# Performance work log

Hardware: AMD Instinct MI355X
Metric: run time of the kernel (lower is better)

## Reference

```python
import jax, jax.numpy as jnp
import numpy as np

GROUP_SIZE = 128

def _dequant(q, s, zp):
    # q: [out, in] int values in [0, 2^bits); s, zp: [out, in//GROUP_SIZE]
    out_dim, in_dim = q.shape
    g = s.shape[1]
    qf = q.reshape(out_dim, g, GROUP_SIZE).astype(s.dtype)
    zf = zp[:, :, None].astype(s.dtype)
    return ((qf - zf) * s[:, :, None]).reshape(out_dim, in_dim)

def setup_inputs() -> dict:
    key = jax.random.key(0)
    ks = jax.random.split(key, 10)
    H, I = 4096, 11008
    T = 64  # decode-like token count -> weight-traffic bound
    gH, gI = H // GROUP_SIZE, I // GROUP_SIZE  # 32, 86
    x = jax.random.normal(ks[0], (T, H), dtype=jnp.float32)
    q1 = jax.random.randint(ks[1], (I, H), 0, 16, dtype=jnp.int32)
    s1 = jax.random.uniform(ks[2], (I, gH), dtype=jnp.float32) * 0.05
    zp1 = jax.random.randint(ks[3], (I, gH), 0, 16, dtype=jnp.int32)
    q3 = jax.random.randint(ks[4], (I, H), 0, 16, dtype=jnp.int32)
    s3 = jax.random.uniform(ks[5], (I, gH), dtype=jnp.float32) * 0.05
    zp3 = jax.random.randint(ks[6], (I, gH), 0, 16, dtype=jnp.int32)
    q2 = jax.random.randint(ks[7], (H, I), 0, 16, dtype=jnp.int32)
    s2 = jax.random.uniform(ks[8], (H, gI), dtype=jnp.float32) * 0.05
    zp2 = jax.random.randint(ks[9], (H, gI), 0, 16, dtype=jnp.int32)
    return {"x": x, "q1": q1, "s1": s1, "zp1": zp1, "q3": q3, "s3": s3,
            "zp3": zp3, "q2": q2, "s2": s2, "zp2": zp2}

def reference(x, q1, s1, zp1, q3, s3, zp3, q2, s2, zp2):
    w1 = _dequant(q1, s1, zp1)  # [I, H]
    w3 = _dequant(q3, s3, zp3)  # [I, H]
    w2 = _dequant(q2, s2, zp2)  # [H, I]
    x1 = x @ w1.T               # [T, I]
    x3 = x @ w3.T               # [T, I]
    x13 = jax.nn.silu(x1) * x3  # OPMX.silu(x1, x3): silu gate times up-proj
    return x13 @ w2.T           # [T, H]
```

## Files before the change

kernel.cpp:

```cpp
#include <hip/hip_runtime.h>
#include <hip/hip_fp16.h>

typedef _Float16 f16;
typedef f16 f16x8 __attribute__((ext_vector_type(8)));
typedef float f32x4 __attribute__((ext_vector_type(4)));

constexpr int T = 64;
constexpr int H = 4096;
constexpr int I = 11008;
constexpr int GH = 32;
constexpr int GI = 86;

__device__ __forceinline__ void gll16(const void* g, void* l) {
    __builtin_amdgcn_global_load_lds(
        (const __attribute__((address_space(1))) unsigned int*)g,
        (__attribute__((address_space(3))) unsigned int*)l, 16, 0, 0);
}

__device__ __forceinline__ f16x8 dq8v(int4 a, int4 b, float sv, float zv) {
    f16x8 r;
    auto p0 = __builtin_amdgcn_cvt_pkrtz((float)a.x * sv - zv, (float)a.y * sv - zv);
    auto p1 = __builtin_amdgcn_cvt_pkrtz((float)a.z * sv - zv, (float)a.w * sv - zv);
    auto p2 = __builtin_amdgcn_cvt_pkrtz((float)b.x * sv - zv, (float)b.y * sv - zv);
    auto p3 = __builtin_amdgcn_cvt_pkrtz((float)b.z * sv - zv, (float)b.w * sv - zv);
    r[0] = p0[0]; r[1] = p0[1]; r[2] = p1[0]; r[3] = p1[1];
    r[4] = p2[0]; r[5] = p2[1]; r[6] = p3[0]; r[7] = p3[1];
    return r;
}

__global__ __launch_bounds__(256) void k_cvt(const float* __restrict__ x,
                                             f16* __restrict__ xp) {
    int C = blockIdx.x * 256 + threadIdx.x;
    int w = C >> 8, m = (C >> 2) & 63, hi = C & 3;
    const float* src = x + (size_t)m * H + w * 32 + hi * 8;
    float4 a = *(const float4*)src;
    float4 b = *(const float4*)(src + 4);
    f16x8 o;
    o[0] = (f16)a.x; o[1] = (f16)a.y; o[2] = (f16)a.z; o[3] = (f16)a.w;
    o[4] = (f16)b.x; o[5] = (f16)b.y; o[6] = (f16)b.z; o[7] = (f16)b.w;
    *(f16x8*)(xp + (size_t)C * 8) = o;
}

__global__ __launch_bounds__(512, 4) void k_gateup(
    const f16* __restrict__ xp,
    const int* __restrict__ q1, const float* __restrict__ s1, const int* __restrict__ zp1,
    const int* __restrict__ q3, const float* __restrict__ s3, const int* __restrict__ zp3,
    float* __restrict__ part)
{
    __shared__ int tile[2 * 8192];
    const int t = threadIdx.x;
    const int wv = t >> 6, lane = t & 63, lo = lane & 15, hi = lane >> 4;
    const int mat = wv & 1, nsub = wv >> 1;
    const int R0 = blockIdx.x * 64;
    const int ks = blockIdx.y;
    const int brow = nsub * 16 + lo;
    const int grow = R0 + brow;
    const float* sm = mat ? s3 : s1;
    const int*   zm = mat ? zp3 : zp1;

    f32x4 acc[4] = {};

    for (int gl = 0; gl < 8; ++gl) {
        int g = ks * 8 + gl;
        float sv = sm[(size_t)grow * GH + g];
        float zv = (float)zm[(size_t)grow * GH + g] * sv;

        __syncthreads();
        #pragma unroll
        for (int k4 = 0; k4 < 4; ++k4) {
            int P = t + k4 * 512;
            int row = P >> 5, c = P & 31, cs = c ^ (row & 7);
            size_t gb = (size_t)(R0 + row) * (H * 4) + (size_t)g * 512 + cs * 16;
            int ldsi = (wv * 64 + k4 * 512) * 4;
            gll16((const char*)q1 + gb, (void*)&tile[ldsi]);
            gll16((const char*)q3 + gb, (void*)&tile[8192 + ldsi]);
        }
        asm volatile("s_waitcnt vmcnt(0)" ::: "memory");
        __syncthreads();

        #pragma unroll
        for (int w = 0; w < 4; ++w) {
            int cc = (w * 8 + hi * 2) ^ (brow & 7);
            int byte0 = mat * 32768 + (brow * 32 + cc) * 16;
            int4 b0 = *(const int4*)((const char*)tile + byte0);
            int4 b1 = *(const int4*)((const char*)tile + (byte0 ^ 16));
            f16x8 bf = dq8v(b0, b1, sv, zv);
            int wg = g * 4 + w;
            #pragma unroll
            for (int mt = 0; mt < 4; ++mt) {
                f16x8 af = *(const f16x8*)(xp + ((size_t)wg * 256 + (mt * 16 + lo) * 4 + hi) * 8);
                acc[mt] = __builtin_amdgcn_mfma_f32_16x16x32_f16(af, bf, acc[mt], 0, 0, 0);
            }
        }
    }

    float* pb = part + (size_t)(ks * 2 + mat) * T * I;
    #pragma unroll
    for (int mt = 0; mt < 4; ++mt)
        #pragma unroll
        for (int j = 0; j < 4; ++j)
            pb[(size_t)(mt * 16 + hi * 4 + j) * I + R0 + brow] = acc[mt][j];
}

__global__ __launch_bounds__(256) void k_comb(const float* __restrict__ part,
                                              f16* __restrict__ hp) {
    int C = blockIdx.x * 256 + threadIdx.x;
    int w = C >> 8, m = (C >> 2) & 63, hi = C & 3;
    int col = w * 32 + hi * 8;
    float ga[8] = {}, ua[8] = {};
    #pragma unroll
    for (int ks = 0; ks < 4; ++ks) {
        const float* pg = part + ((size_t)(ks * 2 + 0) * T + m) * I + col;
        const float* pu = part + ((size_t)(ks * 2 + 1) * T + m) * I + col;
        float4 g0 = *(const float4*)pg, g1 = *(const float4*)(pg + 4);
        float4 u0 = *(const float4*)pu, u1 = *(const float4*)(pu + 4);
        ga[0] += g0.x; ga[1] += g0.y; ga[2] += g0.z; ga[3] += g0.w;
        ga[4] += g1.x; ga[5] += g1.y; ga[6] += g1.z; ga[7] += g1.w;
        ua[0] += u0.x; ua[1] += u0.y; ua[2] += u0.z; ua[3] += u0.w;
        ua[4] += u1.x; ua[5] += u1.y; ua[6] += u1.z; ua[7] += u1.w;
    }
    f16x8 o;
    #pragma unroll
    for (int j = 0; j < 8; ++j) {
        float gv = ga[j];
        o[j] = (f16)(gv / (1.f + __expf(-gv)) * ua[j]);
    }
    *(f16x8*)(hp + (size_t)C * 8) = o;
}

__global__ __launch_bounds__(512, 4) void k_down(
    const f16* __restrict__ hp,
    const int* __restrict__ q2, const float* __restrict__ s2, const int* __restrict__ zp2,
    float* __restrict__ part2)
{
    __shared__ int tile[8192];
    __shared__ float xs[4][64][17];
    const int t = threadIdx.x;
    const int wv = t >> 6, lane = t & 63, lo = lane & 15, hi = lane >> 4;
    const int nsub = wv & 3, kh = wv >> 2;
    const int R0 = blockIdx.x * 64;
    const int y = blockIdx.y;
    const int g0 = (y * GI) >> 3, g1 = ((y + 1) * GI) >> 3;
    const int brow = nsub * 16 + lo;
    const int grow = R0 + brow;

    f32x4 acc[4] = {};

    for (int g = g0; g < g1; ++g) {
        float sv = s2[(size_t)grow * GI + g];
        float zv = (float)zp2[(size_t)grow * GI + g] * sv;

        __syncthreads();
        #pragma unroll
        for (int k4 = 0; k4 < 4; ++k4) {
            int P = t + k4 * 512;
            int row = P >> 5, c = P & 31, cs = c ^ (row & 7);
            size_t gb = (size_t)(R0 + row) * ((size_t)I * 4) + (size_t)g * 512 + cs * 16;
            gll16((const char*)q2 + gb, (void*)&tile[(wv * 64 + k4 * 512) * 4]);
        }
        asm volatile("s_waitcnt vmcnt(0)" ::: "memory");
        __syncthreads();

        #pragma unroll
        for (int ww = 0; ww < 2; ++ww) {
            int w = kh * 2 + ww;
            int cc = (w * 8 + hi * 2) ^ (brow & 7);
            int byte0 = (brow * 32 + cc) * 16;
            int4 b0 = *(const int4*)((const char*)tile + byte0);
            int4 b1 = *(const int4*)((const char*)tile + (byte0 ^ 16));
            f16x8 bf = dq8v(b0, b1, sv, zv);
            int wg = g * 4 + w;
            #pragma unroll
            for (int mt = 0; mt < 4; ++mt) {
                f16x8 af = *(const f16x8*)(hp + ((size_t)wg * 256 + (mt * 16 + lo) * 4 + hi) * 8);
                acc[mt] = __builtin_amdgcn_mfma_f32_16x16x32_f16(af, bf, acc[mt], 0, 0, 0);
            }
        }
    }

    __syncthreads();
    if (kh == 1) {
        #pragma unroll
        for (int mt = 0; mt < 4; ++mt)
            #pragma unroll
            for (int j = 0; j < 4; ++j)
                xs[nsub][mt * 16 + hi * 4 + j][lo] = acc[mt][j];
    }
    __syncthreads();
    if (kh == 0) {
        float* pb = part2 + (size_t)y * T * H;
        #pragma unroll
        for (int mt = 0; mt < 4; ++mt)
            #pragma unroll
            for (int j = 0; j < 4; ++j) {
                int m = mt * 16 + hi * 4 + j;
                pb[(size_t)m * H + R0 + brow] = acc[mt][j] + xs[nsub][m][lo];
            }
    }
}

__global__ __launch_bounds__(256) void k_red(const float* __restrict__ part2,
                                             float* __restrict__ out) {
    int i = (blockIdx.x * 256 + threadIdx.x) * 4;
    float4 s = {0.f, 0.f, 0.f, 0.f};
    #pragma unroll
    for (int y = 0; y < 8; ++y) {
        float4 v = *(const float4*)(part2 + (size_t)y * T * H + i);
        s.x += v.x; s.y += v.y; s.z += v.z; s.w += v.w;
    }
    *(float4*)(out + i) = s;
}

extern "C" void kernel_launch(void* const* d_in, const int* in_sizes, int n_in,
                              void* d_out, int out_size, void* d_ws, size_t ws_size,
                              hipStream_t stream) {
    const float* x   = (const float*)d_in[0];
    const int*   q1  = (const int*)d_in[1];
    const float* s1  = (const float*)d_in[2];
    const int*   zp1 = (const int*)d_in[3];
    const int*   q3  = (const int*)d_in[4];
    const float* s3  = (const float*)d_in[5];
    const int*   zp3 = (const int*)d_in[6];
    const int*   q2  = (const int*)d_in[7];
    const float* s2  = (const float*)d_in[8];
    const int*   zp2 = (const int*)d_in[9];

    char* ws = (char*)d_ws;
    f16*   xp    = (f16*)ws;
    f16*   hp    = (f16*)(ws + 524288);
    float* part  = (float*)(ws + 524288 + 1409024);
    float* part2 = (float*)(ws + 524288 + 1409024 + 22544384);

    k_cvt<<<128, 256, 0, stream>>>(x, xp);
    k_gateup<<<dim3(172, 4), 512, 0, stream>>>(xp, q1, s1, zp1, q3, s3, zp3, part);
    k_comb<<<344, 256, 0, stream>>>(part, hp);
    k_down<<<dim3(64, 8), 512, 0, stream>>>(hp, q2, s2, zp2, part2);
    k_red<<<256, 256, 0, stream>>>(part2, (float*)d_out);
}
```

Measured before the change: 171.8 us.

## Double-buffer weight tiles and split gate/up matrices across grid blocks

Both GEMM kernels now use two LDS buffers so the global-to-LDS load of the next group's weights is issued before the current group is dequantized and multiplied, with a partial vmcnt wait in place of a full drain. Gate and up projections move to separate blocks along a new grid z dimension, and blocks shrink from 512 to 256 threads. The activation fragments for a whole group are preloaded into registers. In k_down the intra-block K split and its LDS reduction are removed. The cost is more registers and LDS per block and fewer waves per block. In k_down each block now does more serial work per output tile.

```diff
diff --git a/kernel.cpp b/kernel.cpp
--- a/kernel.cpp
+++ b/kernel.cpp
@@ -41,57 +41,77 @@
     *(f16x8*)(xp + (size_t)C * 8) = o;
 }
 
-__global__ __launch_bounds__(512, 4) void k_gateup(
+template<int KDIM>
+__device__ __forceinline__ void stage_tile(const int* __restrict__ q, int R0, int g,
+                                           int* buf) {
+    const int t = threadIdx.x;
+    #pragma unroll
+    for (int k4 = 0; k4 < 8; ++k4) {
+        int P = t + k4 * 256;
+        int row = P >> 5, c = P & 31, cs = c ^ (row & 7);
+        size_t gb = (size_t)(R0 + row) * ((size_t)KDIM * 4) + (size_t)g * 512 + cs * 16;
+        gll16((const char*)q + gb, (void*)&buf[((t >> 6) * 64 + k4 * 256) * 4]);
+    }
+}
+
+__global__ __launch_bounds__(256, 2) void k_gateup(
     const f16* __restrict__ xp,
     const int* __restrict__ q1, const float* __restrict__ s1, const int* __restrict__ zp1,
     const int* __restrict__ q3, const float* __restrict__ s3, const int* __restrict__ zp3,
     float* __restrict__ part)
 {
-    __shared__ int tile[2 * 8192];
+    __shared__ int tile[2][8192];
     const int t = threadIdx.x;
     const int wv = t >> 6, lane = t & 63, lo = lane & 15, hi = lane >> 4;
-    const int mat = wv & 1, nsub = wv >> 1;
     const int R0 = blockIdx.x * 64;
     const int ks = blockIdx.y;
-    const int brow = nsub * 16 + lo;
+    const int mat = blockIdx.z;
+    const int brow = wv * 16 + lo;
     const int grow = R0 + brow;
+
+    const int*   q  = mat ? q3 : q1;
     const float* sm = mat ? s3 : s1;
     const int*   zm = mat ? zp3 : zp1;
 
     f32x4 acc[4] = {};
+    int cur = 0;
+
+    stage_tile<H>(q, R0, ks * 8, tile[0]);
 
     for (int gl = 0; gl < 8; ++gl) {
         int g = ks * 8 + gl;
         float sv = sm[(size_t)grow * GH + g];
         float zv = (float)zm[(size_t)grow * GH + g] * sv;
 
-        __syncthreads();
-        #pragma unroll
-        for (int k4 = 0; k4 < 4; ++k4) {
-            int P = t + k4 * 512;
-            int row = P >> 5, c = P & 31, cs = c ^ (row & 7);
-            size_t gb = (size_t)(R0 + row) * (H * 4) + (size_t)g * 512 + cs * 16;
-            int ldsi = (wv * 64 + k4 * 512) * 4;
-            gll16((const char*)q1 + gb, (void*)&tile[ldsi]);
-            gll16((const char*)q3 + gb, (void*)&tile[8192 + ldsi]);
-        }
-        asm volatile("s_waitcnt vmcnt(0)" ::: "memory");
-        __syncthreads();
-
+        f16x8 areg[16];
+        #pragma unroll
+        for (int w = 0; w < 4; ++w)
+            #pragma unroll
+            for (int mt = 0; mt < 4; ++mt)
+                areg[w * 4 + mt] = *(const f16x8*)(xp +
+                    ((size_t)(g * 4 + w) * 256 + (mt * 16 + lo) * 4 + hi) * 8);
+        asm volatile("" ::: "memory");
+
+        int gn = (gl < 7) ? g + 1 : g;
+        stage_tile<H>(q, R0, gn, tile[cur ^ 1]);
+
+        asm volatile("s_waitcnt vmcnt(8)" ::: "memory");
+        __syncthreads();
+
+        const char* tb = (const char*)tile[cur];
         #pragma unroll
         for (int w = 0; w < 4; ++w) {
             int cc = (w * 8 + hi * 2) ^ (brow & 7);
-            int byte0 = mat * 32768 + (brow * 32 + cc) * 16;
-            int4 b0 = *(const int4*)((const char*)tile + byte0);
-            int4 b1 = *(const int4*)((const char*)tile + (byte0 ^ 16));
+            int byte0 = (brow * 32 + cc) * 16;
+            int4 b0 = *(const int4*)(tb + byte0);
+            int4 b1 = *(const int4*)(tb + (byte0 ^ 16));
             f16x8 bf = dq8v(b0, b1, sv, zv);
-            int wg = g * 4 + w;
-            #pragma unroll
-            for (int mt = 0; mt < 4; ++mt) {
-                f16x8 af = *(const f16x8*)(xp + ((size_t)wg * 256 + (mt * 16 + lo) * 4 + hi) * 8);
-                acc[mt] = __builtin_amdgcn_mfma_f32_16x16x32_f16(af, bf, acc[mt], 0, 0, 0);
-            }
+            #pragma unroll
+            for (int mt = 0; mt < 4; ++mt)
+                acc[mt] = __builtin_amdgcn_mfma_f32_16x16x32_f16(areg[w * 4 + mt], bf, acc[mt], 0, 0, 0);
         }
+        __syncthreads();
+        cur ^= 1;
     }
 
     float* pb = part + (size_t)(ks * 2 + mat) * T * I;
@@ -128,75 +148,66 @@
     *(f16x8*)(hp + (size_t)C * 8) = o;
 }
 
-__global__ __launch_bounds__(512, 4) void k_down(
+__global__ __launch_bounds__(256, 2) void k_down(
     const f16* __restrict__ hp,
     const int* __restrict__ q2, const float* __restrict__ s2, const int* __restrict__ zp2,
     float* __restrict__ part2)
 {
-    __shared__ int tile[8192];
-    __shared__ float xs[4][64][17];
+    __shared__ int tile[2][8192];
     const int t = threadIdx.x;
     const int wv = t >> 6, lane = t & 63, lo = lane & 15, hi = lane >> 4;
-    const int nsub = wv & 3, kh = wv >> 2;
     const int R0 = blockIdx.x * 64;
     const int y = blockIdx.y;
     const int g0 = (y * GI) >> 3, g1 = ((y + 1) * GI) >> 3;
-    const int brow = nsub * 16 + lo;
+    const int brow = wv * 16 + lo;
     const int grow = R0 + brow;
 
     f32x4 acc[4] = {};
+    int cur = 0;
+
+    stage_tile<I>(q2, R0, g0, tile[0]);
 
     for (int g = g0; g < g1; ++g) {
         float sv = s2[(size_t)grow * GI + g];
         float zv = (float)zp2[(size_t)grow * GI + g] * sv;
 
-        __syncthreads();
-        #pragma unroll
-        for (int k4 = 0; k4 < 4; ++k4) {
-            int P = t + k4 * 512;
-            int row = P >> 5, c = P & 31, cs = c ^ (row & 7);
-            size_t gb = (size_t)(R0 + row) * ((size_t)I * 4) + (size_t)g * 512 + cs * 16;
-            gll16((const char*)q2 + gb, (void*)&tile[(wv * 64 + k4 * 512) * 4]);
-        }
-        asm volatile("s_waitcnt vmcnt(0)" ::: "memory");
-        __syncthreads();
-
-        #pragma unroll
-        for (int ww = 0; ww < 2; ++ww) {
-            int w = kh * 2 + ww;
+        f16x8 areg[16];
+        #pragma unroll
+        for (int w = 0; w < 4; ++w)
+            #pragma unroll
+            for (int mt = 0; mt < 4; ++mt)
+                areg[w * 4 + mt] = *(const f16x8*)(hp +
+                    ((size_t)(g * 4 + w) * 256 + (mt * 16 + lo) * 4 + hi) * 8);
+        asm volatile("" ::: "memory");
+
+        int gn = (g + 1 < g1) ? g + 1 : g;
+        stage_tile<I>(q2, R0, gn, tile[cur ^ 1]);
+
+        asm volatile("s_waitcnt vmcnt(8)" ::: "memory");
+        __syncthreads();
+
+        const char* tb = (const char*)tile[cur];
+        #pragma unroll
+        for (int w = 0; w < 4; ++w) {
             int cc = (w * 8 + hi * 2) ^ (brow & 7);
             int byte0 = (brow * 32 + cc) * 16;
-            int4 b0 = *(const int4*)((const char*)tile + byte0);
-            int4 b1 = *(const int4*)((const char*)tile + (byte0 ^ 16));
+            int4 b0 = *(const int4*)(tb + byte0);
+            int4 b1 = *(const int4*)(tb + (byte0 ^ 16));
             f16x8 bf = dq8v(b0, b1, sv, zv);
-            int wg = g * 4 + w;
-            #pragma unroll
-            for (int mt = 0; mt < 4; ++mt) {
-                f16x8 af = *(const f16x8*)(hp + ((size_t)wg * 256 + (mt * 16 + lo) * 4 + hi) * 8);
-                acc[mt] = __builtin_amdgcn_mfma_f32_16x16x32_f16(af, bf, acc[mt], 0, 0, 0);
-            }
+            #pragma unroll
+            for (int mt = 0; mt < 4; ++mt)
+                acc[mt] = __builtin_amdgcn_mfma_f32_16x16x32_f16(areg[w * 4 + mt], bf, acc[mt], 0, 0, 0);
         }
-    }
-
-    __syncthreads();
-    if (kh == 1) {
-        #pragma unroll
-        for (int mt = 0; mt < 4; ++mt)
-            #pragma unroll
-            for (int j = 0; j < 4; ++j)
-                xs[nsub][mt * 16 + hi * 4 + j][lo] = acc[mt][j];
-    }
-    __syncthreads();
-    if (kh == 0) {
-        float* pb = part2 + (size_t)y * T * H;
-        #pragma unroll
-        for (int mt = 0; mt < 4; ++mt)
-            #pragma unroll
-            for (int j = 0; j < 4; ++j) {
-                int m = mt * 16 + hi * 4 + j;
-                pb[(size_t)m * H + R0 + brow] = acc[mt][j] + xs[nsub][m][lo];
-            }
-    }
+        __syncthreads();
+        cur ^= 1;
+    }
+
+    float* pb = part2 + (size_t)y * T * H;
+    #pragma unroll
+    for (int mt = 0; mt < 4; ++mt)
+        #pragma unroll
+        for (int j = 0; j < 4; ++j)
+            pb[(size_t)(mt * 16 + hi * 4 + j) * H + R0 + brow] = acc[mt][j];
 }
 
 __global__ __launch_bounds__(256) void k_red(const float* __restrict__ part2,
@@ -232,8 +243,8 @@
     float* part2 = (float*)(ws + 524288 + 1409024 + 22544384);
 
     k_cvt<<<128, 256, 0, stream>>>(x, xp);
-    k_gateup<<<dim3(172, 4), 512, 0, stream>>>(xp, q1, s1, zp1, q3, s3, zp3, part);
+    k_gateup<<<dim3(172, 4, 2), 256, 0, stream>>>(xp, q1, s1, zp1, q3, s3, zp3, part);
     k_comb<<<344, 256, 0, stream>>>(part, hp);
-    k_down<<<dim3(64, 8), 512, 0, stream>>>(hp, q2, s2, zp2, part2);
+    k_down<<<dim3(64, 8), 256, 0, stream>>>(hp, q2, s2, zp2, part2);
     k_red<<<256, 256, 0, stream>>>(part2, (float*)d_out);
 }
```

Result: no change. 174.5 us (+1.6%).

## Re-tile gate/up and down GEMMs into small 16-row blocks with one-shot tile loads

Applied to the files above, without the earlier changes.

Both weight-streaming kernels now use 256-thread blocks that own only 16 output rows. Each block loads its whole K-slice of int32 weights into LDS in one burst instead of a per-group load/sync loop. The K slice is split across the four waves, and their partial results are reduced through shared memory. The grids grow to many more blocks (gate and up are split by matrix on the z axis, and down uses 11 K-splits with an uneven tail), which should expose more memory parallelism for the bandwidth-bound weight reads. The cost is more partial-sum traffic in the final reduction and lower occupancy per block from the larger LDS tile.

```diff
diff --git a/kernel.cpp b/kernel.cpp
--- a/kernel.cpp
+++ b/kernel.cpp
@@ -41,65 +41,75 @@
     *(f16x8*)(xp + (size_t)C * 8) = o;
 }
 
-__global__ __launch_bounds__(512, 4) void k_gateup(
+__global__ __launch_bounds__(256, 2) void k_gateup(
     const f16* __restrict__ xp,
     const int* __restrict__ q1, const float* __restrict__ s1, const int* __restrict__ zp1,
     const int* __restrict__ q3, const float* __restrict__ s3, const int* __restrict__ zp3,
     float* __restrict__ part)
 {
-    __shared__ int tile[2 * 8192];
+    __shared__ int tile[16384];
+    __shared__ float xs[4][64][16];
     const int t = threadIdx.x;
     const int wv = t >> 6, lane = t & 63, lo = lane & 15, hi = lane >> 4;
-    const int mat = wv & 1, nsub = wv >> 1;
-    const int R0 = blockIdx.x * 64;
-    const int ks = blockIdx.y;
-    const int brow = nsub * 16 + lo;
-    const int grow = R0 + brow;
+    const int R0 = blockIdx.x * 16;
+    const int by = blockIdx.y;
+    const int mat = blockIdx.z;
+
+    const int*   q  = mat ? q3 : q1;
     const float* sm = mat ? s3 : s1;
     const int*   zm = mat ? zp3 : zp1;
 
+    #pragma unroll
+    for (int p = 0; p < 16; ++p) {
+        size_t gb = (size_t)(R0 + p) * 16384 + (size_t)by * 4096
+                  + ((t >> 5) * 512) + (((t & 31) ^ (p & 7)) * 16);
+        gll16((const char*)q + gb, (void*)(tile + p * 1024 + wv * 256));
+    }
+    asm volatile("s_waitcnt vmcnt(0)" ::: "memory");
+    __syncthreads();
+
+    const int grow = R0 + lo;
     f32x4 acc[4] = {};
 
-    for (int gl = 0; gl < 8; ++gl) {
-        int g = ks * 8 + gl;
-        float sv = sm[(size_t)grow * GH + g];
-        float zv = (float)zm[(size_t)grow * GH + g] * sv;
-
-        __syncthreads();
-        #pragma unroll
-        for (int k4 = 0; k4 < 4; ++k4) {
-            int P = t + k4 * 512;
-            int row = P >> 5, c = P & 31, cs = c ^ (row & 7);
-            size_t gb = (size_t)(R0 + row) * (H * 4) + (size_t)g * 512 + cs * 16;
-            int ldsi = (wv * 64 + k4 * 512) * 4;
-            gll16((const char*)q1 + gb, (void*)&tile[ldsi]);
-            gll16((const char*)q3 + gb, (void*)&tile[8192 + ldsi]);
+    #pragma unroll
+    for (int s = 0; s < 8; ++s) {
+        int kk = wv * 8 + s;
+        int gg = by * 8 + (kk >> 2);
+        float sv = sm[(size_t)grow * GH + gg];
+        float zv = (float)zm[(size_t)grow * GH + gg] * sv;
+
+        int gG = kk * 8 + hi * 2;
+        int gl = (gG & ~31) | ((gG & 31) ^ (lo & 7));
+        int byte0 = lo * 4096 + gl * 16;
+        const char* tb = (const char*)tile;
+        int4 b0 = *(const int4*)(tb + byte0);
+        int4 b1 = *(const int4*)(tb + (byte0 ^ 16));
+        f16x8 bf = dq8v(b0, b1, sv, zv);
+
+        int kkg = by * 32 + kk;
+        #pragma unroll
+        for (int mt = 0; mt < 4; ++mt) {
+            f16x8 af = *(const f16x8*)(xp +
+                ((size_t)kkg * 256 + (mt * 16 + lo) * 4 + hi) * 8);
+            acc[mt] = __builtin_amdgcn_mfma_f32_16x16x32_f16(af, bf, acc[mt], 0, 0, 0);
         }
-        asm volatile("s_waitcnt vmcnt(0)" ::: "memory");
-        __syncthreads();
-
-        #pragma unroll
-        for (int w = 0; w < 4; ++w) {
-            int cc = (w * 8 + hi * 2) ^ (brow & 7);
-            int byte0 = mat * 32768 + (brow * 32 + cc) * 16;
-            int4 b0 = *(const int4*)((const char*)tile + byte0);
-            int4 b1 = *(const int4*)((const char*)tile + (byte0 ^ 16));
-            f16x8 bf = dq8v(b0, b1, sv, zv);
-            int wg = g * 4 + w;
-            #pragma unroll
-            for (int mt = 0; mt < 4; ++mt) {
-                f16x8 af = *(const f16x8*)(xp + ((size_t)wg * 256 + (mt * 16 + lo) * 4 + hi) * 8);
-                acc[mt] = __builtin_amdgcn_mfma_f32_16x16x32_f16(af, bf, acc[mt], 0, 0, 0);
-            }
-        }
-    }
-
-    float* pb = part + (size_t)(ks * 2 + mat) * T * I;
+    }
+
     #pragma unroll
     for (int mt = 0; mt < 4; ++mt)
         #pragma unroll
         for (int j = 0; j < 4; ++j)
-            pb[(size_t)(mt * 16 + hi * 4 + j) * I + R0 + brow] = acc[mt][j];
+            xs[wv][mt * 16 + hi * 4 + j][lo] = acc[mt][j];
+    __syncthreads();
+
+    float* pb = part + (size_t)(by * 2 + mat) * T * I;
+    #pragma unroll
+    for (int i = 0; i < 4; ++i) {
+        int idx = t + i * 256;
+        int m = idx >> 4, c = idx & 15;
+        float v = xs[0][m][c] + xs[1][m][c] + xs[2][m][c] + xs[3][m][c];
+        pb[(size_t)m * I + R0 + c] = v;
+    }
 }
 
 __global__ __launch_bounds__(256) void k_comb(const float* __restrict__ part,
@@ -128,74 +138,71 @@
     *(f16x8*)(hp + (size_t)C * 8) = o;
 }
 
-__global__ __launch_bounds__(512, 4) void k_down(
+__global__ __launch_bounds__(256, 2) void k_down(
     const f16* __restrict__ hp,
     const int* __restrict__ q2, const float* __restrict__ s2, const int* __restrict__ zp2,
     float* __restrict__ part2)
 {
-    __shared__ int tile[8192];
-    __shared__ float xs[4][64][17];
+    __shared__ int tile[16384];
+    __shared__ float xs[4][64][16];
     const int t = threadIdx.x;
     const int wv = t >> 6, lane = t & 63, lo = lane & 15, hi = lane >> 4;
-    const int nsub = wv & 3, kh = wv >> 2;
-    const int R0 = blockIdx.x * 64;
-    const int y = blockIdx.y;
-    const int g0 = (y * GI) >> 3, g1 = ((y + 1) * GI) >> 3;
-    const int brow = nsub * 16 + lo;
-    const int grow = R0 + brow;
-
+    const int R0 = blockIdx.x * 16;
+    const int by = blockIdx.y;
+    const int CNT = (by < 10) ? 8 : 6;
+    const int rowpitch = CNT * 128;
+
+    if (wv < (CNT >> 1)) {
+        #pragma unroll
+        for (int p = 0; p < 16; ++p) {
+            size_t gb = (size_t)(R0 + p) * 44032 + (size_t)by * 4096
+                      + ((t >> 5) * 512) + (((t & 31) ^ (p & 7)) * 16);
+            gll16((const char*)q2 + gb, (void*)(tile + p * rowpitch + wv * 256));
+        }
+    }
+    asm volatile("s_waitcnt vmcnt(0)" ::: "memory");
+    __syncthreads();
+
+    const int grow = R0 + lo;
     f32x4 acc[4] = {};
 
-    for (int g = g0; g < g1; ++g) {
-        float sv = s2[(size_t)grow * GI + g];
-        float zv = (float)zp2[(size_t)grow * GI + g] * sv;
-
-        __syncthreads();
-        #pragma unroll
-        for (int k4 = 0; k4 < 4; ++k4) {
-            int P = t + k4 * 512;
-            int row = P >> 5, c = P & 31, cs = c ^ (row & 7);
-            size_t gb = (size_t)(R0 + row) * ((size_t)I * 4) + (size_t)g * 512 + cs * 16;
-            gll16((const char*)q2 + gb, (void*)&tile[(wv * 64 + k4 * 512) * 4]);
+    for (int s = 0; s < CNT; ++s) {
+        int kk = wv * CNT + s;
+        int gg = by * 8 + (kk >> 2);
+        float sv = s2[(size_t)grow * GI + gg];
+        float zv = (float)zp2[(size_t)grow * GI + gg] * sv;
+
+        int gG = kk * 8 + hi * 2;
+        int gl = (gG & ~31) | ((gG & 31) ^ (lo & 7));
+        int byte0 = lo * (CNT * 512) + gl * 16;
+        const char* tb = (const char*)tile;
+        int4 b0 = *(const int4*)(tb + byte0);
+        int4 b1 = *(const int4*)(tb + (byte0 ^ 16));
+        f16x8 bf = dq8v(b0, b1, sv, zv);
+
+        int kkg = by * 32 + kk;
+        #pragma unroll
+        for (int mt = 0; mt < 4; ++mt) {
+            f16x8 af = *(const f16x8*)(hp +
+                ((size_t)kkg * 256 + (mt * 16 + lo) * 4 + hi) * 8);
+            acc[mt] = __builtin_amdgcn_mfma_f32_16x16x32_f16(af, bf, acc[mt], 0, 0, 0);
         }
-        asm volatile("s_waitcnt vmcnt(0)" ::: "memory");
-        __syncthreads();
-
-        #pragma unroll
-        for (int ww = 0; ww < 2; ++ww) {
-            int w = kh * 2 + ww;
-            int cc = (w * 8 + hi * 2) ^ (brow & 7);
-            int byte0 = (brow * 32 + cc) * 16;
-            int4 b0 = *(const int4*)((const char*)tile + byte0);
-            int4 b1 = *(const int4*)((const char*)tile + (byte0 ^ 16));
-            f16x8 bf = dq8v(b0, b1, sv, zv);
-            int wg = g * 4 + w;
-            #pragma unroll
-            for (int mt = 0; mt < 4; ++mt) {
-                f16x8 af = *(const f16x8*)(hp + ((size_t)wg * 256 + (mt * 16 + lo) * 4 + hi) * 8);
-                acc[mt] = __builtin_amdgcn_mfma_f32_16x16x32_f16(af, bf, acc[mt], 0, 0, 0);
-            }
-        }
-    }
-
-    __syncthreads();
-    if (kh == 1) {
-        #pragma unroll
-        for (int mt = 0; mt < 4; ++mt)
-            #pragma unroll
-            for (int j = 0; j < 4; ++j)
-                xs[nsub][mt * 16 + hi * 4 + j][lo] = acc[mt][j];
-    }
-    __syncthreads();
-    if (kh == 0) {
-        float* pb = part2 + (size_t)y * T * H;
-        #pragma unroll
-        for (int mt = 0; mt < 4; ++mt)
-            #pragma unroll
-            for (int j = 0; j < 4; ++j) {
-                int m = mt * 16 + hi * 4 + j;
-                pb[(size_t)m * H + R0 + brow] = acc[mt][j] + xs[nsub][m][lo];
-            }
+    }
+
+    #pragma unroll
+    for (int mt = 0; mt < 4; ++mt)
+        #pragma unroll
+        for (int j = 0; j < 4; ++j)
+            xs[wv][mt * 16 + hi * 4 + j][lo] = acc[mt][j];
+    __syncthreads();
+
+    float* pb = part2 + (size_t)by * T * H;
+    #pragma unroll
+    for (int i = 0; i < 4; ++i) {
+        int idx = t + i * 256;
+        int m = idx >> 4, c = idx & 15;
+        float v = xs[0][m][c] + xs[1][m][c] + xs[2][m][c] + xs[3][m][c];
+        pb[(size_t)m * H + R0 + c] = v;
     }
 }
 
@@ -204,7 +211,7 @@
     int i = (blockIdx.x * 256 + threadIdx.x) * 4;
     float4 s = {0.f, 0.f, 0.f, 0.f};
     #pragma unroll
-    for (int y = 0; y < 8; ++y) {
+    for (int y = 0; y < 11; ++y) {
         float4 v = *(const float4*)(part2 + (size_t)y * T * H + i);
         s.x += v.x; s.y += v.y; s.z += v.z; s.w += v.w;
     }
@@ -228,12 +235,12 @@
     char* ws = (char*)d_ws;
     f16*   xp    = (f16*)ws;
     f16*   hp    = (f16*)(ws + 524288);
-    float* part  = (float*)(ws + 524288 + 1409024);
-    float* part2 = (float*)(ws + 524288 + 1409024 + 22544384);
+    float* part  = (float*)(ws + 1933312);
+    float* part2 = (float*)(ws + 24477696);
 
     k_cvt<<<128, 256, 0, stream>>>(x, xp);
-    k_gateup<<<dim3(172, 4), 512, 0, stream>>>(xp, q1, s1, zp1, q3, s3, zp3, part);
+    k_gateup<<<dim3(688, 4, 2), 256, 0, stream>>>(xp, q1, s1, zp1, q3, s3, zp3, part);
     k_comb<<<344, 256, 0, stream>>>(part, hp);
-    k_down<<<dim3(64, 8), 512, 0, stream>>>(hp, q2, s2, zp2, part2);
+    k_down<<<dim3(256, 11), 256, 0, stream>>>(hp, q2, s2, zp2, part2);
     k_red<<<256, 256, 0, stream>>>(part2, (float*)d_out);
 }
```

Result: slower. 216.5 us (+26.1%).
